# Performance work log

Hardware: AMD Instinct MI355X
Metric: run time of the kernel (lower is better)

Reference implementation:

```python
import jax, jax.numpy as jnp
import numpy as np
from jax import lax

B, N, C = 2, 4096, 128
HEADS = 4
HD = C // HEADS
EXP = 2  # FFN_expand
EPS = 1e-5


def layernorm(x, w, b):
    mu = jnp.mean(x, axis=-1, keepdims=True)
    var = jnp.mean(jnp.square(x - mu), axis=-1, keepdims=True)
    return (x - mu) * lax.rsqrt(var + EPS) * w + b


def conv2d(x, w, b, pad, groups=1):
    # x: [B, Cin, H, W], w: [Cout, Cin//groups, kh, kw]
    y = lax.conv_general_dilated(
        x, w, window_strides=(1, 1), padding=[(pad, pad), (pad, pad)],
        dimension_numbers=('NCHW', 'OIHW', 'NCHW'), feature_group_count=groups)
    return y + b[None, :, None, None]


def setup_inputs() -> dict:
    key = jax.random.key(0)
    ks = jax.random.split(key, 16)
    C2 = C * EXP
    inp = {
        'x': jax.random.normal(ks[0], (B, N, C), jnp.float32),
        'H': 64,
        'W': 64,
        'ln1_w': jnp.ones((C,), jnp.float32),
        'ln1_b': jnp.zeros((C,), jnp.float32),
        'q_w': jax.random.normal(ks[1], (C, C), jnp.float32) * 0.02,
        'kv_w': jax.random.normal(ks[2], (2 * C, C), jnp.float32) * 0.02,
        'proj_w': jax.random.normal(ks[3], (C, C), jnp.float32) * 0.02,
        'proj_b': jnp.zeros((C,), jnp.float32),
        'ln2_w': jnp.ones((C,), jnp.float32),
        'ln2_b': jnp.zeros((C,), jnp.float32),
        'conv1_w': jax.random.normal(ks[4], (C2, C, 1, 1), jnp.float32) * np.sqrt(2.0 / C2),
        'conv1_b': jnp.zeros((C2,), jnp.float32),
        'conv33_w': jax.random.normal(ks[5], (C2, 1, 3, 3), jnp.float32) * np.sqrt(2.0 / 9),
        'conv33_b': jnp.zeros((C2,), jnp.float32),
        'conv55_w': jax.random.normal(ks[6], (C2, 1, 5, 5), jnp.float32) * np.sqrt(2.0 / 25),
        'conv55_b': jnp.zeros((C2,), jnp.float32),
        'conv4_w': jax.random.normal(ks[7], (C, C, 1, 1), jnp.float32) * np.sqrt(2.0 / C),
        'conv4_b': jnp.zeros((C,), jnp.float32),
    }
    return inp


def reference(x, H, W, ln1_w, ln1_b, q_w, kv_w, proj_w, proj_b,
              ln2_w, ln2_b, conv1_w, conv1_b, conv33_w, conv33_b,
              conv55_w, conv55_b, conv4_w, conv4_b):
    b, n, c = x.shape
    scale = HD ** -0.5

    # ---- Multi-head self-attention (sr_ratio=1) ----
    h = layernorm(x, ln1_w, ln1_b)
    q = jnp.einsum('bnc,oc->bno', h, q_w).reshape(b, n, HEADS, HD).transpose(0, 2, 1, 3)
    kv = jnp.einsum('bnc,oc->bno', h, kv_w).reshape(b, n, 2, HEADS, HD).transpose(2, 0, 3, 1, 4)
    k, v = kv[0], kv[1]
    attn = jnp.einsum('bhqd,bhkd->bhqk', q, k) * scale  # [B, heads, N, N]
    attn = jax.nn.softmax(attn, axis=-1)
    out = jnp.einsum('bhqk,bhkd->bhqd', attn, v).transpose(0, 2, 1, 3).reshape(b, n, c)
    out = jnp.einsum('bnc,oc->bno', out, proj_w) + proj_b
    x = x + out

    # ---- MFFN: conv1 + (dw3x3 + dw5x5) branches, SimpleGate, conv4 ----
    h = layernorm(x, ln2_w, ln2_b)
    hc = h.reshape(b, H, W, c).transpose(0, 3, 1, 2)  # NCHW
    x1 = conv2d(hc, conv1_w, conv1_b, pad=0)
    x33 = conv2d(x1, conv33_w, conv33_b, pad=1, groups=c * EXP)
    x55 = conv2d(x1, conv55_w, conv55_b, pad=2, groups=c * EXP)
    s = x1 + x33 + x55
    a, g = jnp.split(s, 2, axis=1)  # SimpleGate
    gated = a * g
    y = conv2d(gated, conv4_w, conv4_b, pad=0)
    y = y.transpose(0, 2, 3, 1).reshape(b, H * W, c)
    return x + y
```

## Files before the change

### kernel.cpp

```cpp
#include <hip/hip_runtime.h>
#include <hip/hip_bf16.h>
#include <math.h>

#define NB 2
#define NN 4096
#define NC 128
#define NH 4
#define HD 32
#define C2 256
#define HW 64
#define EPS 1e-5f

typedef unsigned short u16;
typedef short bf16x8 __attribute__((ext_vector_type(8)));
typedef unsigned short u16x8 __attribute__((ext_vector_type(8)));
typedef float f32x16 __attribute__((ext_vector_type(16)));

__device__ __forceinline__ u16 f2b(float x) {
    return __bfloat16_as_ushort(__float2bfloat16(x));
}
__device__ __forceinline__ float b2f(u16 v) {
    return __uint_as_float((unsigned)v << 16);
}
__device__ __forceinline__ unsigned pack_bf16(float a, float b) {
    return (unsigned)f2b(a) | ((unsigned)f2b(b) << 16);
}
__device__ __forceinline__ f32x16 fzero16() {
    f32x16 z;
    #pragma unroll
    for (int i = 0; i < 16; ++i) z[i] = 0.f;
    return z;
}
union U32x4 { unsigned u[4]; bf16x8 v; };

__device__ __forceinline__ void plswap(unsigned& a, unsigned& b) {
    asm("v_permlane32_swap_b32 %0, %1" : "+v"(a), "+v"(b));
}
__device__ __forceinline__ float xswap(float v, int h5) {
    float a = v, b = v;
    asm("v_permlane32_swap_b32 %0, %1" : "+v"(a), "+v"(b));
    return h5 ? a : b;
}

__global__ __launch_bounds__(256) void k_prep_ln(
    const float* __restrict__ q_w, const float* __restrict__ kv_w,
    const float* __restrict__ proj_w, const float* __restrict__ c1_w,
    const float* __restrict__ c4_w, const float* __restrict__ c33_w,
    const float* __restrict__ c55_w, const float* __restrict__ c33_b,
    const float* __restrict__ c55_b,
    u16* wqkv, u16* wproj, u16* wc1, u16* wc4,
    u16* weff, float* beff,
    const float* __restrict__ x, const float* __restrict__ ln1w,
    const float* __restrict__ ln1b, u16* __restrict__ h1) {
    if (blockIdx.x < 2048) {
        const int l = threadIdx.x & 63, wid = threadIdx.x >> 6;
        const int row = blockIdx.x * 4 + wid;
        const float2 xv = *(const float2*)(x + (size_t)row * NC + l * 2);
        float sum = xv.x + xv.y, ss = xv.x * xv.x + xv.y * xv.y;
        #pragma unroll
        for (int off = 1; off < 64; off <<= 1) {
            sum += __shfl_xor(sum, off);
            ss  += __shfl_xor(ss, off);
        }
        const float mean = sum * (1.0f / NC);
        const float var  = ss * (1.0f / NC) - mean * mean;
        const float rstd = rsqrtf(var + EPS);
        const float2 wv = *(const float2*)(ln1w + l * 2);
        const float2 bv = *(const float2*)(ln1b + l * 2);
        const float h0 = (xv.x - mean) * rstd * wv.x + bv.x;
        const float h1v = (xv.y - mean) * rstd * wv.y + bv.y;
        *(unsigned*)(h1 + (size_t)row * NC + l * 2) = pack_bf16(h0, h1v);
        return;
    }
    const int tid = (blockIdx.x - 2048) * 256 + threadIdx.x;
    const int nth = 64 * 256;
    const float s = 0.17677669529663687f * 1.4426950408889634f;
    for (int i = tid; i < 128 * 128; i += nth) wqkv[i] = f2b(q_w[i] * s);
    for (int i = tid; i < 256 * 128; i += nth) wqkv[128 * 128 + i] = f2b(kv_w[i]);
    for (int i = tid; i < 128 * 128; i += nth) wproj[i] = f2b(proj_w[i]);
    for (int i = tid; i < 256 * 128; i += nth) wc1[i] = f2b(c1_w[i]);
    for (int i = tid; i < 128 * 128; i += nth) wc4[i] = f2b(c4_w[i]);
    for (int i = tid; i < 25 * 256; i += nth) {
        const int k = i / 256, c = i % 256;
        const int dy = k / 5 - 2, dx = k % 5 - 2;
        float w = c55_w[c * 25 + k];
        if (dy >= -1 && dy <= 1 && dx >= -1 && dx <= 1)
            w += c33_w[c * 9 + (dy + 1) * 3 + (dx + 1)];
        if (k == 12) w += 1.0f;
        weff[k * 256 + c] = f2b(w);
    }
    for (int i = tid; i < 256; i += nth) beff[i] = c33_b[i] + c55_b[i];
}

__device__ __forceinline__ f32x16 gemm_tile_32x32(
    const u16* __restrict__ A, const u16* __restrict__ W, int m0, int n0, int q, int h5) {
    const u16* ap = A + (size_t)(m0 + q) * 128 + h5 * 8;
    const u16* wp = W + (size_t)(n0 + q) * 128 + h5 * 8;
    f32x16 acc = fzero16();
    #pragma unroll
    for (int kk = 0; kk < 8; ++kk) {
        bf16x8 af = *(const bf16x8*)(ap + kk * 16);
        bf16x8 wf = *(const bf16x8*)(wp + kk * 16);
        acc = __builtin_amdgcn_mfma_f32_32x32x16_bf16(af, wf, acc, 0, 0, 0);
    }
    return acc;
}
#define GEMM_PROLOG(NCOLS)                                    \
    const int l = threadIdx.x & 63, wid = threadIdx.x >> 6;   \
    const int q = l & 31, h5 = l >> 5;                        \
    const int m0 = blockIdx.x * 64 + (wid >> 1) * 32;         \
    const int n0 = blockIdx.y * 64 + (wid & 1) * 32;          \
    const int o = n0 + q;                                     \
    (void)o;

__global__ __launch_bounds__(256) void k_gemm_qkv(
    const u16* __restrict__ h1, const u16* __restrict__ wqkv,
    u16* __restrict__ qb, u16* __restrict__ kbuf, u16* __restrict__ vtb) {
    GEMM_PROLOG(384)
    f32x16 acc = gemm_tile_32x32(h1, wqkv, m0, n0, q, h5);
    if (o < 256) {
        #pragma unroll
        for (int r = 0; r < 16; ++r) {
            const int mr = m0 + (r & 3) + 8 * (r >> 2) + 4 * h5;
            const int b_ = mr >> 12, n = mr & 4095;
            const u16 val = f2b(acc[r]);
            if (o < 128) {
                qb[((size_t)(b_ * 4 + (o >> 5)) * NN + n) * HD + (o & 31)] = val;
            } else {
                const int o2 = o - 128;
                kbuf[((size_t)(b_ * 4 + (o2 >> 5)) * NN + n) * HD + (o2 & 31)] = val;
            }
        }
    } else {
        const int vo = o - 256;
        const int hh = vo >> 5, d = vo & 31;
        u16* vrow = vtb + ((size_t)((m0 >> 12) * 4 + hh) * 32 + d) * NN;
        const int nb = (m0 & 4095) + 4 * h5;
        #pragma unroll
        for (int g = 0; g < 4; ++g) {
            ushort4 pv;
            pv.x = f2b(acc[4 * g + 0]); pv.y = f2b(acc[4 * g + 1]);
            pv.z = f2b(acc[4 * g + 2]); pv.w = f2b(acc[4 * g + 3]);
            *(ushort4*)(vrow + nb + 8 * g) = pv;
        }
    }
}

__global__ __launch_bounds__(256, 4) void k_attn(
    const u16* __restrict__ qb, const u16* __restrict__ kbuf, const u16* __restrict__ vtb,
    u16* __restrict__ ctxb) {
    __shared__ float sl[4][32];
    __shared__ float so[4][64][17];

    const int l = threadIdx.x & 63, w = threadIdx.x >> 6;
    const int q = l & 31, h5 = l >> 5;
    const int bh = blockIdx.x;
    const int qbase = blockIdx.y * 32;

    const u16* qp = qb + ((size_t)bh * NN + qbase + q) * HD + h5 * 8;
    const bf16x8 qf0 = *(const bf16x8*)qp;
    const bf16x8 qf1 = *(const bf16x8*)(qp + 16);

    const int kb0 = w * 1024;
    const u16* kp = kbuf + ((size_t)bh * NN + kb0 + q) * HD + h5 * 8;
    const u16* vp = vtb + ((size_t)bh * 32 + q) * NN + kb0 + h5 * 8;

    f32x16 O = fzero16();
    float lacc = 0.f;

    bf16x8 kf0 = *(const bf16x8*)kp;
    bf16x8 kf1 = *(const bf16x8*)(kp + 16);
    bf16x8 vf0 = *(const bf16x8*)vp;
    bf16x8 vf1 = *(const bf16x8*)(vp + 16);

    for (int t = 0; t < 32; ++t) {
        const u16* kpn = kp + ((t < 31) ? 32 * HD : 0);
        const u16* vpn = vp + ((t < 31) ? 32 : 0);
        const bf16x8 nk0 = *(const bf16x8*)kpn;
        const bf16x8 nk1 = *(const bf16x8*)(kpn + 16);
        const bf16x8 nv0 = *(const bf16x8*)vpn;
        const bf16x8 nv1 = *(const bf16x8*)(vpn + 16);

        f32x16 s = fzero16();
        s = __builtin_amdgcn_mfma_f32_32x32x16_bf16(kf0, qf0, s, 0, 0, 0);
        s = __builtin_amdgcn_mfma_f32_32x32x16_bf16(kf1, qf1, s, 0, 0, 0);

        float p[16];
        #pragma unroll
        for (int r = 0; r < 16; ++r) p[r] = __builtin_amdgcn_exp2f(s[r]);

        {
            const float s0 = (p[0] + p[1]) + (p[2] + p[3]);
            const float s1 = (p[4] + p[5]) + (p[6] + p[7]);
            const float s2 = (p[8] + p[9]) + (p[10] + p[11]);
            const float s3 = (p[12] + p[13]) + (p[14] + p[15]);
            float ls = (s0 + s1) + (s2 + s3);
            ls += xswap(ls, h5);
            lacc += ls;
        }

        unsigned pk[8];
        #pragma unroll
        for (int i = 0; i < 8; ++i) pk[i] = pack_bf16(p[2 * i], p[2 * i + 1]);
        U32x4 a0, a1;
        {
            unsigned x0 = pk[0], x2 = pk[2]; plswap(x0, x2);
            unsigned x1 = pk[1], x3 = pk[3]; plswap(x1, x3);
            a0.u[0] = x0; a0.u[1] = x1; a0.u[2] = x2; a0.u[3] = x3;
            unsigned y0 = pk[4], y2 = pk[6]; plswap(y0, y2);
            unsigned y1 = pk[5], y3 = pk[7]; plswap(y1, y3);
            a1.u[0] = y0; a1.u[1] = y1; a1.u[2] = y2; a1.u[3] = y3;
        }
        O = __builtin_amdgcn_mfma_f32_32x32x16_bf16(a0.v, vf0, O, 0, 0, 0);
        O = __builtin_amdgcn_mfma_f32_32x32x16_bf16(a1.v, vf1, O, 0, 0, 0);

        kf0 = nk0; kf1 = nk1; vf0 = nv0; vf1 = nv1;
        kp = kpn; vp = vpn;
    }

    if (l < 32) sl[w][l] = lacc;
    #pragma unroll
    for (int r = 0; r < 16; ++r) so[w][l][r] = O[r];
    __syncthreads();

    const int b_ = bh >> 2, h_ = bh & 3;
    #pragma unroll
    for (int i = 0; i < 4; ++i) {
        const int r = 4 * w + i;
        const int qr = (r & 3) + 8 * (r >> 2) + 4 * h5;
        const float os = so[0][l][r] + so[1][l][r] + so[2][l][r] + so[3][l][r];
        const float Lq = sl[0][qr] + sl[1][qr] + sl[2][qr] + sl[3][qr];
        ctxb[((size_t)(b_ * NN + qbase + qr)) * NC + h_ * 32 + q] = f2b(os / Lq);
    }
}

__global__ __launch_bounds__(256) void k_proj_ln(
    const u16* __restrict__ ctxb, const u16* __restrict__ wproj,
    const float* __restrict__ pbias, const float* __restrict__ x,
    const float* __restrict__ lnw, const float* __restrict__ lnb,
    float* __restrict__ x2, u16* __restrict__ h2) {
    __shared__ float sx[32][129];
    const int l = threadIdx.x & 63, wid = threadIdx.x >> 6;
    const int q = l & 31, h5 = l >> 5;
    const int m0 = blockIdx.x * 32;
    const int n0 = wid * 32;
    const int o = n0 + q;

    f32x16 acc = gemm_tile_32x32(ctxb, wproj, m0, n0, q, h5);
    const float bo = pbias[o];
    #pragma unroll
    for (int r = 0; r < 16; ++r) {
        const int rr = (r & 3) + 8 * (r >> 2) + 4 * h5;
        const int mr = m0 + rr;
        const float xv = acc[r] + bo + x[(size_t)mr * NC + o];
        x2[(size_t)mr * NC + o] = xv;
        sx[rr][o] = xv;
    }
    __syncthreads();

    const int t = threadIdx.x;
    const int row = t >> 3, cs = (t & 7) * 16;
    float vals[16];
    float sum = 0.f, ss = 0.f;
    #pragma unroll
    for (int i = 0; i < 16; ++i) {
        const float v = sx[row][cs + i];
        vals[i] = v; sum += v; ss += v * v;
    }
    #pragma unroll
    for (int off = 1; off < 8; off <<= 1) {
        sum += __shfl_xor(sum, off);
        ss  += __shfl_xor(ss, off);
    }
    const float mean = sum * (1.0f / NC);
    const float var  = ss * (1.0f / NC) - mean * mean;
    const float rstd = rsqrtf(var + EPS);
    const size_t base = (size_t)(m0 + row) * NC + cs;
    #pragma unroll
    for (int i = 0; i < 16; i += 2) {
        const float h0 = (vals[i]     - mean) * rstd * lnw[cs + i]     + lnb[cs + i];
        const float h1 = (vals[i + 1] - mean) * rstd * lnw[cs + i + 1] + lnb[cs + i + 1];
        *(unsigned*)(h2 + base + i) = pack_bf16(h0, h1);
    }
}

__global__ __launch_bounds__(256) void k_gemm_c1(
    const u16* __restrict__ h2, const u16* __restrict__ wc1,
    const float* __restrict__ bias, u16* __restrict__ x1) {
    GEMM_PROLOG(256)
    f32x16 acc = gemm_tile_32x32(h2, wc1, m0, n0, q, h5);
    const float bo = bias[o];
    #pragma unroll
    for (int r = 0; r < 16; ++r) {
        const int mr = m0 + (r & 3) + 8 * (r >> 2) + 4 * h5;
        x1[(size_t)mr * 256 + o] = f2b(acc[r] + bo);
    }
}

template<bool CHK>
__device__ __forceinline__ void dw_accum(
    const u16* __restrict__ base, const u16* __restrict__ weff,
    int py, int px, int cg,
    float& a0, float& a1, float& a2, float& a3,
    float& g0, float& g1, float& g2, float& g3) {
    #pragma unroll
    for (int dy = -2; dy <= 2; ++dy) {
        const int yy = py + dy;
        const bool yin = !CHK || ((yy >= 0) && (yy < HW));
        #pragma unroll
        for (int dx = -2; dx <= 2; ++dx) {
            const int xx = px + dx;
            const bool in = !CHK || (yin && (xx >= 0) && (xx < HW));
            const int k5 = (dy + 2) * 5 + (dx + 2);
            const u16* xp = base + (dy * HW + dx) * C2;
            ushort4 xa = in ? *(const ushort4*)(xp + cg) : ushort4{0, 0, 0, 0};
            ushort4 xg = in ? *(const ushort4*)(xp + 128 + cg) : ushort4{0, 0, 0, 0};
            const ushort4 wa = *(const ushort4*)(weff + k5 * 256 + cg);
            const ushort4 wg = *(const ushort4*)(weff + k5 * 256 + 128 + cg);
            a0 += b2f(xa.x) * b2f(wa.x); a1 += b2f(xa.y) * b2f(wa.y);
            a2 += b2f(xa.z) * b2f(wa.z); a3 += b2f(xa.w) * b2f(wa.w);
            g0 += b2f(xg.x) * b2f(wg.x); g1 += b2f(xg.y) * b2f(wg.y);
            g2 += b2f(xg.z) * b2f(wg.z); g3 += b2f(xg.w) * b2f(wg.w);
        }
    }
}

__global__ __launch_bounds__(256) void k_dwgate(
    const u16* __restrict__ x1, const u16* __restrict__ weff, const float* __restrict__ beff,
    u16* __restrict__ gatedb) {
    const int t = threadIdx.x;
    const int cg = (t & 31) * 4;
    const int pb = blockIdx.x * 8 + (t >> 5);
    const int b_ = pb >> 12, p = pb & 4095;
    const int py = p >> 6, px = p & 63;
    const int px0 = (blockIdx.x * 8) & 63;
    const u16* base = x1 + ((size_t)b_ * 4096 + p) * C2;

    float a0 = 0.f, a1 = 0.f, a2 = 0.f, a3 = 0.f;
    float g0 = 0.f, g1 = 0.f, g2 = 0.f, g3 = 0.f;
    const bool interior = (py >= 2) && (py < 62) && (px0 >= 8) && (px0 <= 48);
    if (interior) {
        dw_accum<false>(base, weff, py, px, cg, a0, a1, a2, a3, g0, g1, g2, g3);
    } else {
        dw_accum<true>(base, weff, py, px, cg, a0, a1, a2, a3, g0, g1, g2, g3);
    }
    const float4 ba = *(const float4*)(beff + cg);
    const float4 bg = *(const float4*)(beff + 128 + cg);
    ushort4 o4;
    o4.x = f2b((a0 + ba.x) * (g0 + bg.x));
    o4.y = f2b((a1 + ba.y) * (g1 + bg.y));
    o4.z = f2b((a2 + ba.z) * (g2 + bg.z));
    o4.w = f2b((a3 + ba.w) * (g3 + bg.w));
    *(ushort4*)(gatedb + (size_t)pb * 128 + cg) = o4;
}

__global__ __launch_bounds__(256) void k_gemm_c4(
    const u16* __restrict__ gatedb, const u16* __restrict__ wc4,
    const float* __restrict__ bias, const float* __restrict__ x2, float* __restrict__ out) {
    GEMM_PROLOG(128)
    f32x16 acc = gemm_tile_32x32(gatedb, wc4, m0, n0, q, h5);
    const float bo = bias[o];
    #pragma unroll
    for (int r = 0; r < 16; ++r) {
        const int mr = m0 + (r & 3) + 8 * (r >> 2) + 4 * h5;
        out[(size_t)mr * 128 + o] = acc[r] + bo + x2[(size_t)mr * 128 + o];
    }
}

extern "C" void kernel_launch(void* const* d_in, const int* in_sizes, int n_in,
                              void* d_out, int out_size, void* d_ws, size_t ws_size,
                              hipStream_t stream) {
    const float* x      = (const float*)d_in[0];
    const float* ln1_w  = (const float*)d_in[3];
    const float* ln1_b  = (const float*)d_in[4];
    const float* q_w    = (const float*)d_in[5];
    const float* kv_w   = (const float*)d_in[6];
    const float* proj_w = (const float*)d_in[7];
    const float* proj_b = (const float*)d_in[8];
    const float* ln2_w  = (const float*)d_in[9];
    const float* ln2_b  = (const float*)d_in[10];
    const float* c1_w   = (const float*)d_in[11];
    const float* c1_b   = (const float*)d_in[12];
    const float* c33_w  = (const float*)d_in[13];
    const float* c33_b  = (const float*)d_in[14];
    const float* c55_w  = (const float*)d_in[15];
    const float* c55_b  = (const float*)d_in[16];
    const float* c4_w   = (const float*)d_in[17];
    const float* c4_b   = (const float*)d_in[18];

    char* p = (char*)d_ws;
    u16*   wqkv  = (u16*)p;   p += 384 * 128 * 2;
    u16*   wproj = (u16*)p;   p += 128 * 128 * 2;
    u16*   wc1   = (u16*)p;   p += 256 * 128 * 2;
    u16*   wc4   = (u16*)p;   p += 128 * 128 * 2;
    u16*   weff  = (u16*)p;   p += 25 * 256 * 2;
    float* beff  = (float*)p; p += 256 * 4;
    p = (char*)(((size_t)p + 255) & ~(size_t)255);
    u16*   h1    = (u16*)p;   p += (size_t)8192 * 128 * 2;
    u16*   qb    = (u16*)p;   p += (size_t)8 * 4096 * 32 * 2;
    u16*   kb    = (u16*)p;   p += (size_t)8 * 4096 * 32 * 2;
    u16*   vtb   = (u16*)p;   p += (size_t)8 * 32 * 4096 * 2;
    u16*   ctxb  = (u16*)p;   p += (size_t)8192 * 128 * 2;
    float* x2    = (float*)p; p += (size_t)8192 * 128 * 4;
    u16*   h2    = (u16*)p;   p += (size_t)8192 * 128 * 2;
    u16*   x1    = (u16*)p;   p += (size_t)8192 * 256 * 2;
    u16*   gatedb= (u16*)p;   p += (size_t)8192 * 128 * 2;
    float* out   = (float*)d_out;

    k_prep_ln<<<2112, 256, 0, stream>>>(q_w, kv_w, proj_w, c1_w, c4_w, c33_w, c55_w,
                                        c33_b, c55_b, wqkv, wproj, wc1, wc4, weff, beff,
                                        x, ln1_w, ln1_b, h1);
    k_gemm_qkv<<<dim3(128, 6), 256, 0, stream>>>(h1, wqkv, qb, kb, vtb);
    k_attn<<<dim3(NB * NH, NN / 32), 256, 0, stream>>>(qb, kb, vtb, ctxb);
    k_proj_ln<<<256, 256, 0, stream>>>(ctxb, wproj, proj_b, x, ln2_w, ln2_b, x2, h2);
    k_gemm_c1<<<dim3(128, 4), 256, 0, stream>>>(h2, wc1, c1_b, x1);
    k_dwgate<<<1024, 256, 0, stream>>>(x1, weff, beff, gatedb);
    k_gemm_c4<<<dim3(128, 2), 256, 0, stream>>>(gatedb, wc4, c4_b, x2, out);
}
```

Measured before the change: 220.1 us.

## Fuse proj+LN+conv1 and dwconv+gate+conv4; split attention keys over eight waves

The attention kernel now uses 512-thread blocks, with eight waves each covering 512 keys instead of four waves covering 1024. This shortens each wave's serial loop and raises parallelism, at the cost of a larger shared-memory reduction. The projection, LayerNorm and conv1 GEMM are fused into one kernel that keeps the normalized rows in swizzled LDS. The depthwise conv, gate and conv4 GEMM are fused the same way, which removes the h2 and gated intermediates and two launches. The fused MFFN kernels launch only 256 blocks each, so occupancy may be low.

```diff
diff --git a/kernel.cpp b/kernel.cpp
--- a/kernel.cpp
+++ b/kernel.cpp
@@ -105,18 +105,15 @@
     }
     return acc;
 }
-#define GEMM_PROLOG(NCOLS)                                    \
-    const int l = threadIdx.x & 63, wid = threadIdx.x >> 6;   \
-    const int q = l & 31, h5 = l >> 5;                        \
-    const int m0 = blockIdx.x * 64 + (wid >> 1) * 32;         \
-    const int n0 = blockIdx.y * 64 + (wid & 1) * 32;          \
-    const int o = n0 + q;                                     \
-    (void)o;
 
 __global__ __launch_bounds__(256) void k_gemm_qkv(
     const u16* __restrict__ h1, const u16* __restrict__ wqkv,
     u16* __restrict__ qb, u16* __restrict__ kbuf, u16* __restrict__ vtb) {
-    GEMM_PROLOG(384)
+    const int l = threadIdx.x & 63, wid = threadIdx.x >> 6;
+    const int q = l & 31, h5 = l >> 5;
+    const int m0 = blockIdx.x * 64 + (wid >> 1) * 32;
+    const int n0 = blockIdx.y * 64 + (wid & 1) * 32;
+    const int o = n0 + q;
     f32x16 acc = gemm_tile_32x32(h1, wqkv, m0, n0, q, h5);
     if (o < 256) {
         #pragma unroll
@@ -146,11 +143,11 @@
     }
 }
 
-__global__ __launch_bounds__(256, 4) void k_attn(
+__global__ __launch_bounds__(512) void k_attn(
     const u16* __restrict__ qb, const u16* __restrict__ kbuf, const u16* __restrict__ vtb,
     u16* __restrict__ ctxb) {
-    __shared__ float sl[4][32];
-    __shared__ float so[4][64][17];
+    __shared__ float sl[8][32];
+    __shared__ float so[8][64][17];
 
     const int l = threadIdx.x & 63, w = threadIdx.x >> 6;
     const int q = l & 31, h5 = l >> 5;
@@ -161,7 +158,7 @@
     const bf16x8 qf0 = *(const bf16x8*)qp;
     const bf16x8 qf1 = *(const bf16x8*)(qp + 16);
 
-    const int kb0 = w * 1024;
+    const int kb0 = w * 512;
     const u16* kp = kbuf + ((size_t)bh * NN + kb0 + q) * HD + h5 * 8;
     const u16* vp = vtb + ((size_t)bh * 32 + q) * NN + kb0 + h5 * 8;
 
@@ -173,9 +170,9 @@
     bf16x8 vf0 = *(const bf16x8*)vp;
     bf16x8 vf1 = *(const bf16x8*)(vp + 16);
 
-    for (int t = 0; t < 32; ++t) {
-        const u16* kpn = kp + ((t < 31) ? 32 * HD : 0);
-        const u16* vpn = vp + ((t < 31) ? 32 : 0);
+    for (int t = 0; t < 16; ++t) {
+        const u16* kpn = kp + ((t < 15) ? 32 * HD : 0);
+        const u16* vpn = vp + ((t < 15) ? 32 : 0);
         const bf16x8 nk0 = *(const bf16x8*)kpn;
         const bf16x8 nk1 = *(const bf16x8*)(kpn + 16);
         const bf16x8 nv0 = *(const bf16x8*)vpn;
@@ -225,75 +222,96 @@
 
     const int b_ = bh >> 2, h_ = bh & 3;
     #pragma unroll
-    for (int i = 0; i < 4; ++i) {
-        const int r = 4 * w + i;
+    for (int i = 0; i < 2; ++i) {
+        const int r = 2 * w + i;
         const int qr = (r & 3) + 8 * (r >> 2) + 4 * h5;
-        const float os = so[0][l][r] + so[1][l][r] + so[2][l][r] + so[3][l][r];
-        const float Lq = sl[0][qr] + sl[1][qr] + sl[2][qr] + sl[3][qr];
+        float os = 0.f, Lq = 0.f;
+        #pragma unroll
+        for (int ww = 0; ww < 8; ++ww) {
+            os += so[ww][l][r];
+            Lq += sl[ww][qr];
+        }
         ctxb[((size_t)(b_ * NN + qbase + qr)) * NC + h_ * 32 + q] = f2b(os / Lq);
     }
 }
 
-__global__ __launch_bounds__(256) void k_proj_ln(
+__global__ __launch_bounds__(256) void k_mffn_a(
     const u16* __restrict__ ctxb, const u16* __restrict__ wproj,
     const float* __restrict__ pbias, const float* __restrict__ x,
     const float* __restrict__ lnw, const float* __restrict__ lnb,
-    float* __restrict__ x2, u16* __restrict__ h2) {
+    const u16* __restrict__ wc1, const float* __restrict__ c1b,
+    float* __restrict__ x2, u16* __restrict__ x1) {
     __shared__ float sx[32][129];
+    __shared__ u16 sh2[32][128];
     const int l = threadIdx.x & 63, wid = threadIdx.x >> 6;
     const int q = l & 31, h5 = l >> 5;
     const int m0 = blockIdx.x * 32;
-    const int n0 = wid * 32;
-    const int o = n0 + q;
-
-    f32x16 acc = gemm_tile_32x32(ctxb, wproj, m0, n0, q, h5);
-    const float bo = pbias[o];
-    #pragma unroll
-    for (int r = 0; r < 16; ++r) {
-        const int rr = (r & 3) + 8 * (r >> 2) + 4 * h5;
-        const int mr = m0 + rr;
-        const float xv = acc[r] + bo + x[(size_t)mr * NC + o];
-        x2[(size_t)mr * NC + o] = xv;
-        sx[rr][o] = xv;
+
+    {
+        const int n0 = wid * 32;
+        const int o = n0 + q;
+        f32x16 acc = gemm_tile_32x32(ctxb, wproj, m0, n0, q, h5);
+        const float bo = pbias[o];
+        #pragma unroll
+        for (int r = 0; r < 16; ++r) {
+            const int rr = (r & 3) + 8 * (r >> 2) + 4 * h5;
+            const int mr = m0 + rr;
+            const float xv = acc[r] + bo + x[(size_t)mr * NC + o];
+            x2[(size_t)mr * NC + o] = xv;
+            sx[rr][o] = xv;
+        }
     }
     __syncthreads();
 
-    const int t = threadIdx.x;
-    const int row = t >> 3, cs = (t & 7) * 16;
-    float vals[16];
-    float sum = 0.f, ss = 0.f;
-    #pragma unroll
-    for (int i = 0; i < 16; ++i) {
-        const float v = sx[row][cs + i];
-        vals[i] = v; sum += v; ss += v * v;
-    }
-    #pragma unroll
-    for (int off = 1; off < 8; off <<= 1) {
-        sum += __shfl_xor(sum, off);
-        ss  += __shfl_xor(ss, off);
-    }
-    const float mean = sum * (1.0f / NC);
-    const float var  = ss * (1.0f / NC) - mean * mean;
-    const float rstd = rsqrtf(var + EPS);
-    const size_t base = (size_t)(m0 + row) * NC + cs;
-    #pragma unroll
-    for (int i = 0; i < 16; i += 2) {
-        const float h0 = (vals[i]     - mean) * rstd * lnw[cs + i]     + lnb[cs + i];
-        const float h1 = (vals[i + 1] - mean) * rstd * lnw[cs + i + 1] + lnb[cs + i + 1];
-        *(unsigned*)(h2 + base + i) = pack_bf16(h0, h1);
-    }
-}
-
-__global__ __launch_bounds__(256) void k_gemm_c1(
-    const u16* __restrict__ h2, const u16* __restrict__ wc1,
-    const float* __restrict__ bias, u16* __restrict__ x1) {
-    GEMM_PROLOG(256)
-    f32x16 acc = gemm_tile_32x32(h2, wc1, m0, n0, q, h5);
-    const float bo = bias[o];
-    #pragma unroll
-    for (int r = 0; r < 16; ++r) {
-        const int mr = m0 + (r & 3) + 8 * (r >> 2) + 4 * h5;
-        x1[(size_t)mr * 256 + o] = f2b(acc[r] + bo);
+    {
+        const int t = threadIdx.x;
+        const int row = t >> 3, cs = (t & 7) * 16;
+        float vals[16];
+        float sum = 0.f, ss = 0.f;
+        #pragma unroll
+        for (int i = 0; i < 16; ++i) {
+            const float v = sx[row][cs + i];
+            vals[i] = v; sum += v; ss += v * v;
+        }
+        #pragma unroll
+        for (int off = 1; off < 8; off <<= 1) {
+            sum += __shfl_xor(sum, off);
+            ss  += __shfl_xor(ss, off);
+        }
+        const float mean = sum * (1.0f / NC);
+        const float var  = ss * (1.0f / NC) - mean * mean;
+        const float rstd = rsqrtf(var + EPS);
+        char* rowp = (char*)&sh2[row][0];
+        const int sw = (row & 15) << 4;
+        #pragma unroll
+        for (int i = 0; i < 16; i += 2) {
+            const float h0 = (vals[i]     - mean) * rstd * lnw[cs + i]     + lnb[cs + i];
+            const float h1 = (vals[i + 1] - mean) * rstd * lnw[cs + i + 1] + lnb[cs + i + 1];
+            *(unsigned*)(rowp + (((cs + i) * 2) ^ sw)) = pack_bf16(h0, h1);
+        }
+    }
+    __syncthreads();
+
+    const char* arow = (const char*)&sh2[q][0];
+    const int asw = (q & 15) << 4;
+    #pragma unroll
+    for (int tt = 0; tt < 2; ++tt) {
+        const int n1 = (wid * 2 + tt) * 32;
+        const int o1 = n1 + q;
+        const u16* wp = wc1 + (size_t)o1 * 128 + h5 * 8;
+        f32x16 acc = fzero16();
+        #pragma unroll
+        for (int kk = 0; kk < 8; ++kk) {
+            const bf16x8 af = *(const bf16x8*)(arow + ((h5 * 16 + kk * 32) ^ asw));
+            const bf16x8 wf = *(const bf16x8*)(wp + kk * 16);
+            acc = __builtin_amdgcn_mfma_f32_32x32x16_bf16(af, wf, acc, 0, 0, 0);
+        }
+        const float bo = c1b[o1];
+        #pragma unroll
+        for (int r = 0; r < 16; ++r) {
+            const int mr = m0 + (r & 3) + 8 * (r >> 2) + 4 * h5;
+            x1[(size_t)mr * 256 + o1] = f2b(acc[r] + bo);
+        }
     }
 }
 
@@ -325,44 +343,60 @@
     }
 }
 
-__global__ __launch_bounds__(256) void k_dwgate(
+__global__ __launch_bounds__(256) void k_mffn_b(
     const u16* __restrict__ x1, const u16* __restrict__ weff, const float* __restrict__ beff,
-    u16* __restrict__ gatedb) {
+    const u16* __restrict__ wc4, const float* __restrict__ c4b,
+    const float* __restrict__ x2, float* __restrict__ out) {
+    __shared__ u16 sg[32][128];
     const int t = threadIdx.x;
-    const int cg = (t & 31) * 4;
-    const int pb = blockIdx.x * 8 + (t >> 5);
-    const int b_ = pb >> 12, p = pb & 4095;
-    const int py = p >> 6, px = p & 63;
-    const int px0 = (blockIdx.x * 8) & 63;
-    const u16* base = x1 + ((size_t)b_ * 4096 + p) * C2;
-
-    float a0 = 0.f, a1 = 0.f, a2 = 0.f, a3 = 0.f;
-    float g0 = 0.f, g1 = 0.f, g2 = 0.f, g3 = 0.f;
-    const bool interior = (py >= 2) && (py < 62) && (px0 >= 8) && (px0 <= 48);
-    if (interior) {
-        dw_accum<false>(base, weff, py, px, cg, a0, a1, a2, a3, g0, g1, g2, g3);
-    } else {
-        dw_accum<true>(base, weff, py, px, cg, a0, a1, a2, a3, g0, g1, g2, g3);
-    }
-    const float4 ba = *(const float4*)(beff + cg);
-    const float4 bg = *(const float4*)(beff + 128 + cg);
-    ushort4 o4;
-    o4.x = f2b((a0 + ba.x) * (g0 + bg.x));
-    o4.y = f2b((a1 + ba.y) * (g1 + bg.y));
-    o4.z = f2b((a2 + ba.z) * (g2 + bg.z));
-    o4.w = f2b((a3 + ba.w) * (g3 + bg.w));
-    *(ushort4*)(gatedb + (size_t)pb * 128 + cg) = o4;
-}
-
-__global__ __launch_bounds__(256) void k_gemm_c4(
-    const u16* __restrict__ gatedb, const u16* __restrict__ wc4,
-    const float* __restrict__ bias, const float* __restrict__ x2, float* __restrict__ out) {
-    GEMM_PROLOG(128)
-    f32x16 acc = gemm_tile_32x32(gatedb, wc4, m0, n0, q, h5);
-    const float bo = bias[o];
+    const int pb0 = blockIdx.x * 32;
+
+    #pragma unroll
+    for (int u = 0; u < 4; ++u) {
+        const int unit = t + u * 256;
+        const int pxl = unit >> 5;
+        const int cg = (unit & 31) * 4;
+        const int pb = pb0 + pxl;
+        const int p = pb & 4095;
+        const int py = p >> 6, px = p & 63;
+        const u16* base = x1 + (size_t)pb * C2;
+
+        float a0 = 0.f, a1 = 0.f, a2 = 0.f, a3 = 0.f;
+        float g0 = 0.f, g1 = 0.f, g2 = 0.f, g3 = 0.f;
+        if ((py >= 2) && (py < 62) && (px >= 2) && (px < 62)) {
+            dw_accum<false>(base, weff, py, px, cg, a0, a1, a2, a3, g0, g1, g2, g3);
+        } else {
+            dw_accum<true>(base, weff, py, px, cg, a0, a1, a2, a3, g0, g1, g2, g3);
+        }
+        const float4 ba = *(const float4*)(beff + cg);
+        const float4 bg = *(const float4*)(beff + 128 + cg);
+        ushort4 o4;
+        o4.x = f2b((a0 + ba.x) * (g0 + bg.x));
+        o4.y = f2b((a1 + ba.y) * (g1 + bg.y));
+        o4.z = f2b((a2 + ba.z) * (g2 + bg.z));
+        o4.w = f2b((a3 + ba.w) * (g3 + bg.w));
+        *(ushort4*)((char*)&sg[pxl][0] + ((cg * 2) ^ ((pxl & 15) << 4))) = o4;
+    }
+    __syncthreads();
+
+    const int l = t & 63, wid = t >> 6;
+    const int q = l & 31, h5 = l >> 5;
+    const int n0 = wid * 32;
+    const int o = n0 + q;
+    const char* arow = (const char*)&sg[q][0];
+    const int asw = (q & 15) << 4;
+    const u16* wp = wc4 + (size_t)o * 128 + h5 * 8;
+    f32x16 acc = fzero16();
+    #pragma unroll
+    for (int kk = 0; kk < 8; ++kk) {
+        const bf16x8 af = *(const bf16x8*)(arow + ((h5 * 16 + kk * 32) ^ asw));
+        const bf16x8 wf = *(const bf16x8*)(wp + kk * 16);
+        acc = __builtin_amdgcn_mfma_f32_32x32x16_bf16(af, wf, acc, 0, 0, 0);
+    }
+    const float bo = c4b[o];
     #pragma unroll
     for (int r = 0; r < 16; ++r) {
-        const int mr = m0 + (r & 3) + 8 * (r >> 2) + 4 * h5;
+        const int mr = pb0 + (r & 3) + 8 * (r >> 2) + 4 * h5;
         out[(size_t)mr * 128 + o] = acc[r] + bo + x2[(size_t)mr * 128 + o];
     }
 }
@@ -402,18 +436,15 @@
     u16*   vtb   = (u16*)p;   p += (size_t)8 * 32 * 4096 * 2;
     u16*   ctxb  = (u16*)p;   p += (size_t)8192 * 128 * 2;
     float* x2    = (float*)p; p += (size_t)8192 * 128 * 4;
-    u16*   h2    = (u16*)p;   p += (size_t)8192 * 128 * 2;
     u16*   x1    = (u16*)p;   p += (size_t)8192 * 256 * 2;
-    u16*   gatedb= (u16*)p;   p += (size_t)8192 * 128 * 2;
     float* out   = (float*)d_out;
 
     k_prep_ln<<<2112, 256, 0, stream>>>(q_w, kv_w, proj_w, c1_w, c4_w, c33_w, c55_w,
                                         c33_b, c55_b, wqkv, wproj, wc1, wc4, weff, beff,
                                         x, ln1_w, ln1_b, h1);
     k_gemm_qkv<<<dim3(128, 6), 256, 0, stream>>>(h1, wqkv, qb, kb, vtb);
-    k_attn<<<dim3(NB * NH, NN / 32), 256, 0, stream>>>(qb, kb, vtb, ctxb);
-    k_proj_ln<<<256, 256, 0, stream>>>(ctxb, wproj, proj_b, x, ln2_w, ln2_b, x2, h2);
-    k_gemm_c1<<<dim3(128, 4), 256, 0, stream>>>(h2, wc1, c1_b, x1);
-    k_dwgate<<<1024, 256, 0, stream>>>(x1, weff, beff, gatedb);
-    k_gemm_c4<<<dim3(128, 2), 256, 0, stream>>>(gatedb, wc4, c4_b, x2, out);
-}
+    k_attn<<<dim3(NB * NH, NN / 32), 512, 0, stream>>>(qb, kb, vtb, ctxb);
+    k_mffn_a<<<256, 256, 0, stream>>>(ctxb, wproj, proj_b, x, ln2_w, ln2_b,
+                                      wc1, c1_b, x2, x1);
+    k_mffn_b<<<256, 256, 0, stream>>>(x1, weff, beff, wc4, c4_b, x2, out);
+}
```

New measurement: 217.0 us. Within noise of the previous version (-1.4%).

## Split attention keys across eight waves, shrink GEMM blocks, unfuse proj and LN2

Applied to the files above, without the earlier changes.

The attention kernel now splits the key range across 8 waves of 512 keys each instead of 4 waves of 1024, so each workgroup has more concurrent waves and shorter serial loops, with an 8-way reduction through shared memory at the end. The GEMM kernels switch to 128-thread blocks each covering a 32-row tile, which doubles the grid size. The fused projection+LayerNorm kernel is split into a plain projection GEMM and a separate wave-per-row LN2 kernel. The goal is more parallelism for latency-bound kernels, at the cost of an extra launch, an extra round trip of x2 through memory, and larger shared memory use in attention.

```diff
diff --git a/kernel.cpp b/kernel.cpp
--- a/kernel.cpp
+++ b/kernel.cpp
@@ -105,18 +105,18 @@
     }
     return acc;
 }
-#define GEMM_PROLOG(NCOLS)                                    \
+#define GEMM_PROLOG2()                                        \
     const int l = threadIdx.x & 63, wid = threadIdx.x >> 6;   \
     const int q = l & 31, h5 = l >> 5;                        \
-    const int m0 = blockIdx.x * 64 + (wid >> 1) * 32;         \
-    const int n0 = blockIdx.y * 64 + (wid & 1) * 32;          \
+    const int m0 = blockIdx.x * 32;                           \
+    const int n0 = blockIdx.y * 64 + wid * 32;                \
     const int o = n0 + q;                                     \
     (void)o;
 
-__global__ __launch_bounds__(256) void k_gemm_qkv(
+__global__ __launch_bounds__(128) void k_gemm_qkv(
     const u16* __restrict__ h1, const u16* __restrict__ wqkv,
     u16* __restrict__ qb, u16* __restrict__ kbuf, u16* __restrict__ vtb) {
-    GEMM_PROLOG(384)
+    GEMM_PROLOG2()
     f32x16 acc = gemm_tile_32x32(h1, wqkv, m0, n0, q, h5);
     if (o < 256) {
         #pragma unroll
@@ -146,11 +146,11 @@
     }
 }
 
-__global__ __launch_bounds__(256, 4) void k_attn(
+__global__ __launch_bounds__(512) void k_attn(
     const u16* __restrict__ qb, const u16* __restrict__ kbuf, const u16* __restrict__ vtb,
     u16* __restrict__ ctxb) {
-    __shared__ float sl[4][32];
-    __shared__ float so[4][64][17];
+    __shared__ float sl[8][32];
+    __shared__ float so[8][64][17];
 
     const int l = threadIdx.x & 63, w = threadIdx.x >> 6;
     const int q = l & 31, h5 = l >> 5;
@@ -161,7 +161,7 @@
     const bf16x8 qf0 = *(const bf16x8*)qp;
     const bf16x8 qf1 = *(const bf16x8*)(qp + 16);
 
-    const int kb0 = w * 1024;
+    const int kb0 = w * 512;
     const u16* kp = kbuf + ((size_t)bh * NN + kb0 + q) * HD + h5 * 8;
     const u16* vp = vtb + ((size_t)bh * 32 + q) * NN + kb0 + h5 * 8;
 
@@ -173,9 +173,9 @@
     bf16x8 vf0 = *(const bf16x8*)vp;
     bf16x8 vf1 = *(const bf16x8*)(vp + 16);
 
-    for (int t = 0; t < 32; ++t) {
-        const u16* kpn = kp + ((t < 31) ? 32 * HD : 0);
-        const u16* vpn = vp + ((t < 31) ? 32 : 0);
+    for (int t = 0; t < 16; ++t) {
+        const u16* kpn = kp + ((t < 15) ? 32 * HD : 0);
+        const u16* vpn = vp + ((t < 15) ? 32 : 0);
         const bf16x8 nk0 = *(const bf16x8*)kpn;
         const bf16x8 nk1 = *(const bf16x8*)(kpn + 16);
         const bf16x8 nv0 = *(const bf16x8*)vpn;
@@ -225,69 +225,58 @@
 
     const int b_ = bh >> 2, h_ = bh & 3;
     #pragma unroll
-    for (int i = 0; i < 4; ++i) {
-        const int r = 4 * w + i;
+    for (int i = 0; i < 2; ++i) {
+        const int r = 2 * w + i;
         const int qr = (r & 3) + 8 * (r >> 2) + 4 * h5;
-        const float os = so[0][l][r] + so[1][l][r] + so[2][l][r] + so[3][l][r];
-        const float Lq = sl[0][qr] + sl[1][qr] + sl[2][qr] + sl[3][qr];
+        float os = 0.f, Lq = 0.f;
+        #pragma unroll
+        for (int ww = 0; ww < 8; ++ww) {
+            os += so[ww][l][r];
+            Lq += sl[ww][qr];
+        }
         ctxb[((size_t)(b_ * NN + qbase + qr)) * NC + h_ * 32 + q] = f2b(os / Lq);
     }
 }
 
-__global__ __launch_bounds__(256) void k_proj_ln(
+__global__ __launch_bounds__(128) void k_gemm_proj(
     const u16* __restrict__ ctxb, const u16* __restrict__ wproj,
-    const float* __restrict__ pbias, const float* __restrict__ x,
-    const float* __restrict__ lnw, const float* __restrict__ lnb,
-    float* __restrict__ x2, u16* __restrict__ h2) {
-    __shared__ float sx[32][129];
-    const int l = threadIdx.x & 63, wid = threadIdx.x >> 6;
-    const int q = l & 31, h5 = l >> 5;
-    const int m0 = blockIdx.x * 32;
-    const int n0 = wid * 32;
-    const int o = n0 + q;
-
+    const float* __restrict__ pbias, const float* __restrict__ x, float* __restrict__ x2) {
+    GEMM_PROLOG2()
     f32x16 acc = gemm_tile_32x32(ctxb, wproj, m0, n0, q, h5);
     const float bo = pbias[o];
     #pragma unroll
     for (int r = 0; r < 16; ++r) {
-        const int rr = (r & 3) + 8 * (r >> 2) + 4 * h5;
-        const int mr = m0 + rr;
-        const float xv = acc[r] + bo + x[(size_t)mr * NC + o];
-        x2[(size_t)mr * NC + o] = xv;
-        sx[rr][o] = xv;
-    }
-    __syncthreads();
-
-    const int t = threadIdx.x;
-    const int row = t >> 3, cs = (t & 7) * 16;
-    float vals[16];
-    float sum = 0.f, ss = 0.f;
-    #pragma unroll
-    for (int i = 0; i < 16; ++i) {
-        const float v = sx[row][cs + i];
-        vals[i] = v; sum += v; ss += v * v;
-    }
-    #pragma unroll
-    for (int off = 1; off < 8; off <<= 1) {
+        const int mr = m0 + (r & 3) + 8 * (r >> 2) + 4 * h5;
+        x2[(size_t)mr * 128 + o] = acc[r] + bo + x[(size_t)mr * 128 + o];
+    }
+}
+
+__global__ __launch_bounds__(256) void k_ln2(
+    const float* __restrict__ x, const float* __restrict__ w, const float* __restrict__ b,
+    u16* __restrict__ h) {
+    const int l = threadIdx.x & 63, wid = threadIdx.x >> 6;
+    const int row = blockIdx.x * 4 + wid;
+    const float2 xv = *(const float2*)(x + (size_t)row * NC + l * 2);
+    float sum = xv.x + xv.y, ss = xv.x * xv.x + xv.y * xv.y;
+    #pragma unroll
+    for (int off = 1; off < 64; off <<= 1) {
         sum += __shfl_xor(sum, off);
         ss  += __shfl_xor(ss, off);
     }
     const float mean = sum * (1.0f / NC);
     const float var  = ss * (1.0f / NC) - mean * mean;
     const float rstd = rsqrtf(var + EPS);
-    const size_t base = (size_t)(m0 + row) * NC + cs;
-    #pragma unroll
-    for (int i = 0; i < 16; i += 2) {
-        const float h0 = (vals[i]     - mean) * rstd * lnw[cs + i]     + lnb[cs + i];
-        const float h1 = (vals[i + 1] - mean) * rstd * lnw[cs + i + 1] + lnb[cs + i + 1];
-        *(unsigned*)(h2 + base + i) = pack_bf16(h0, h1);
-    }
-}
-
-__global__ __launch_bounds__(256) void k_gemm_c1(
+    const float2 wv = *(const float2*)(w + l * 2);
+    const float2 bv = *(const float2*)(b + l * 2);
+    const float h0 = (xv.x - mean) * rstd * wv.x + bv.x;
+    const float h1 = (xv.y - mean) * rstd * wv.y + bv.y;
+    *(unsigned*)(h + (size_t)row * NC + l * 2) = pack_bf16(h0, h1);
+}
+
+__global__ __launch_bounds__(128) void k_gemm_c1(
     const u16* __restrict__ h2, const u16* __restrict__ wc1,
     const float* __restrict__ bias, u16* __restrict__ x1) {
-    GEMM_PROLOG(256)
+    GEMM_PROLOG2()
     f32x16 acc = gemm_tile_32x32(h2, wc1, m0, n0, q, h5);
     const float bo = bias[o];
     #pragma unroll
@@ -354,10 +343,10 @@
     *(ushort4*)(gatedb + (size_t)pb * 128 + cg) = o4;
 }
 
-__global__ __launch_bounds__(256) void k_gemm_c4(
+__global__ __launch_bounds__(128) void k_gemm_c4(
     const u16* __restrict__ gatedb, const u16* __restrict__ wc4,
     const float* __restrict__ bias, const float* __restrict__ x2, float* __restrict__ out) {
-    GEMM_PROLOG(128)
+    GEMM_PROLOG2()
     f32x16 acc = gemm_tile_32x32(gatedb, wc4, m0, n0, q, h5);
     const float bo = bias[o];
     #pragma unroll
@@ -410,10 +399,11 @@
     k_prep_ln<<<2112, 256, 0, stream>>>(q_w, kv_w, proj_w, c1_w, c4_w, c33_w, c55_w,
                                         c33_b, c55_b, wqkv, wproj, wc1, wc4, weff, beff,
                                         x, ln1_w, ln1_b, h1);
-    k_gemm_qkv<<<dim3(128, 6), 256, 0, stream>>>(h1, wqkv, qb, kb, vtb);
-    k_attn<<<dim3(NB * NH, NN / 32), 256, 0, stream>>>(qb, kb, vtb, ctxb);
-    k_proj_ln<<<256, 256, 0, stream>>>(ctxb, wproj, proj_b, x, ln2_w, ln2_b, x2, h2);
-    k_gemm_c1<<<dim3(128, 4), 256, 0, stream>>>(h2, wc1, c1_b, x1);
+    k_gemm_qkv<<<dim3(256, 6), 128, 0, stream>>>(h1, wqkv, qb, kb, vtb);
+    k_attn<<<dim3(NB * NH, NN / 32), 512, 0, stream>>>(qb, kb, vtb, ctxb);
+    k_gemm_proj<<<dim3(256, 2), 128, 0, stream>>>(ctxb, wproj, proj_b, x, x2);
+    k_ln2<<<2048, 256, 0, stream>>>(x2, ln2_w, ln2_b, h2);
+    k_gemm_c1<<<dim3(256, 4), 128, 0, stream>>>(h2, wc1, c1_b, x1);
     k_dwgate<<<1024, 256, 0, stream>>>(x1, weff, beff, gatedb);
-    k_gemm_c4<<<dim3(128, 2), 256, 0, stream>>>(gatedb, wc4, c4_b, x2, out);
-}
+    k_gemm_c4<<<dim3(256, 2), 128, 0, stream>>>(gatedb, wc4, c4_b, x2, out);
+}
```

New measurement: 223.5 us. About the same (+1.5%).
